# Kernel optimization log

Measured on AMD Instinct MI355X. Metric: run time of the kernel, lower is better.

Reference implementation:

```python
import jax, jax.numpy as jnp
import numpy as np

N_NODES = 50000
N_EDGES = 1600000
IN_CH = 129   # encoding_dim + node_dim
OUT_CH = 64
PERIODS = 25
N_TRAIN = 25000


def setup_inputs() -> dict:
    key = jax.random.key(0)
    ks = jax.random.split(key, 24)
    inp = {
        'x': jax.random.normal(ks[0], (N_NODES, IN_CH, PERIODS), dtype=jnp.float32),
        'edge_index': jax.random.randint(ks[1], (2, N_EDGES), 0, N_NODES, dtype=jnp.int64),
        'y': jax.random.uniform(ks[2], (N_NODES,), dtype=jnp.float32),
        'train_idx': jax.random.randint(ks[3], (N_TRAIN,), 0, N_NODES, dtype=jnp.int64),
    }
    s_in = 1.0 / np.sqrt(IN_CH)
    s_2o = 1.0 / np.sqrt(2 * OUT_CH)
    s_o = 1.0 / np.sqrt(OUT_CH)
    # TGCN gate params: GCNConv weight/bias (IN_CH->OUT_CH), Linear(2*OUT_CH->OUT_CH)
    names = ['z', 'r', 'h']
    for i, g in enumerate(names):
        inp[f'W_{g}'] = jax.random.uniform(ks[4 + 4 * i], (IN_CH, OUT_CH), minval=-s_in, maxval=s_in)
        inp[f'b_{g}'] = jax.random.uniform(ks[5 + 4 * i], (OUT_CH,), minval=-s_in, maxval=s_in)
        inp[f'Wl_{g}'] = jax.random.uniform(ks[6 + 4 * i], (2 * OUT_CH, OUT_CH), minval=-s_2o, maxval=s_2o)
        inp[f'bl_{g}'] = jax.random.uniform(ks[7 + 4 * i], (OUT_CH,), minval=-s_2o, maxval=s_2o)
    inp['attention'] = jax.random.uniform(ks[16], (PERIODS,), dtype=jnp.float32)
    inp['W_o'] = jax.random.uniform(ks[17], (OUT_CH, 1), minval=-s_o, maxval=s_o)
    inp['b_o'] = jax.random.uniform(ks[18], (1,), minval=-s_o, maxval=s_o)
    return inp


def _forward(x, edge_index, y, train_idx, attention,
             W_z, b_z, Wl_z, bl_z, W_r, b_r, Wl_r, bl_r,
             W_h, b_h, Wl_h, bl_h, W_o, b_o):
    N = x.shape[0]
    src, dst = edge_index[0], edge_index[1]
    # GCN symmetric norm with self-loops (edge_weight = 1)
    deg = 1.0 + jax.ops.segment_sum(jnp.ones_like(src, dtype=x.dtype), dst, num_segments=N)
    dinv = jax.lax.rsqrt(deg)
    edge_norm = (dinv[src] * dinv[dst])[:, None]   # (E,1)
    self_norm = (dinv * dinv)[:, None]              # (N,1)

    def gcn(xt, W, b):
        h = xt @ W                                   # (N, OUT_CH)
        agg = jax.ops.segment_sum(edge_norm * h[src], dst, num_segments=N)
        return agg + self_norm * h + b

    probs = jax.nn.softmax(attention)               # (PERIODS,)
    x_seq = jnp.transpose(x, (2, 0, 1))             # (T, N, IN_CH)

    def step(carry, xp):
        H, acc = carry
        xt, p = xp
        Z = jax.nn.sigmoid(jnp.concatenate([gcn(xt, W_z, b_z), H], axis=1) @ Wl_z + bl_z)
        R = jax.nn.sigmoid(jnp.concatenate([gcn(xt, W_r, b_r), H], axis=1) @ Wl_r + bl_r)
        H_tilde = jnp.tanh(jnp.concatenate([gcn(xt, W_h, b_h), H * R], axis=1) @ Wl_h + bl_h)
        H = Z * H + (1.0 - Z) * H_tilde
        return (H, acc + p * H), None

    H0 = jnp.zeros((N, OUT_CH), dtype=x.dtype)
    (H, H_accum), _ = jax.lax.scan(step, (H0, H0), (x_seq, probs))

    out = jax.nn.sigmoid(H_accum @ W_o + b_o)       # (N, 1)
    y_pred = out[:, 0][train_idx]
    return y_pred, y[train_idx]


def reference(x, edge_index, y, train_idx, attention,
              W_z, b_z, Wl_z, bl_z, W_r, b_r, Wl_r, bl_r,
              W_h, b_h, Wl_h, bl_h, W_o, b_o):
    return _forward(x, edge_index, y, train_idx, attention,
                    W_z, b_z, Wl_z, bl_z, W_r, b_r, Wl_r, bl_r,
                    W_h, b_h, Wl_h, bl_h, W_o, b_o)
```

## Files before the change

### kernel.cpp

```cpp
#include <hip/hip_runtime.h>
#include <stdint.h>

#define NND 50000
#define NNDP 50016
#define NE  1600000
#define INC 129
#define TP  25
#define NTR 25000
#define MPAD 50048
#define NC 192
#define NB_SCAN 196
#define CSR_MAX (NE + 8*NND + 128)

typedef short bf16x8 __attribute__((ext_vector_type(8)));
typedef float f32x4 __attribute__((ext_vector_type(4)));
typedef float f32x2 __attribute__((ext_vector_type(2)));

__device__ __forceinline__ uint32_t f2bf(float f){
  union{float ff; uint32_t u;} v; v.ff=f;
  return (v.u + 0x7FFFu + ((v.u>>16)&1u))>>16;
}
__device__ __forceinline__ uint32_t pack2(float a, float b){
  return f2bf(a) | (f2bf(b)<<16);
}
__device__ __forceinline__ float sigm(float v){ return 1.f/(1.f+__expf(-v)); }

__global__ void k_prep(const float* Wz, const float* bz, const float* Wlz, const float* blz,
                       const float* Wr, const float* br, const float* Wlr, const float* blr,
                       const float* Wh, const float* bh, const float* Wlh, const float* blh,
                       uint16_t* BTf, float* ceff, uint16_t* Wlf)
{
  int idx = blockIdx.x*256 + threadIdx.x;
  if (idx < NC*224) {
    int j = idx / 224, k = idx - j*224;
    int g = j >> 6, jj = j & 63;
    const float* W  = g==0?Wz :(g==1?Wr :Wh);
    const float* Wl = g==0?Wlz:(g==1?Wlr:Wlh);
    float v = 0.f;
    if (k < INC) {
      for (int m=0;m<64;m++) v += W[k*64+m]*Wl[m*64+jj];
    } else if (k >= 160) {
      int kk = k-160;
      v = (g<2) ? Wl[(64+kk)*64 + jj] : 0.f;
    }
    int cc = (j>>4)&3, c16 = j&15;
    int kd = k>>1, kk = kd>>4, kgrp = (kd>>2)&3, dw = kd&3, half = k&1;
    int lane = kgrp*16 + c16;
    BTf[(((g*7+kk)*4+cc)*256 + lane*4 + dw)*2 + half] = (uint16_t)f2bf(v);
  } else if (idx < NC*224 + 64*64) {
    int t = idx - NC*224; int j2 = t>>6, k2 = t&63;
    int cc = j2>>4, c16 = j2&15;
    int kd = k2>>1, kk2 = kd>>4, kgrp = (kd>>2)&3, dw = kd&3, half = k2&1;
    int lane = kgrp*16 + c16;
    Wlf[((kk2*4+cc)*256 + lane*4 + dw)*2 + half] = (uint16_t)f2bf(Wlh[(64+k2)*64 + j2]);
  } else if (idx < NC*224 + 64*64 + NC) {
    int j = idx - NC*224 - 64*64;
    int g = j>>6, jj = j&63;
    const float* b  = g==0?bz :(g==1?br :bh);
    const float* Wl = g==0?Wlz:(g==1?Wlr:Wlh);
    const float* bl = g==0?blz:(g==1?blr:blh);
    float v = bl[jj];
    for (int m=0;m<64;m++) v += b[m]*Wl[m*64+jj];
    ceff[j] = v;
  }
}

__global__ void k_probs(const float* att, float* probs){
  if (threadIdx.x==0 && blockIdx.x==0){
    float m=-1e30f;
    for (int i=0;i<TP;i++) m = fmaxf(m, att[i]);
    float e[TP]; float s=0.f;
    for (int i=0;i<TP;i++){ e[i]=__expf(att[i]-m); s+=e[i]; }
    for (int i=0;i<TP;i++) probs[i]=e[i]/s;
  }
}

__global__ void k_hist(const int* eidx, int* deg){
  int e = blockIdx.x*256 + threadIdx.x;
  if (e < NE) atomicAdd(&deg[eidx[NE + e]], 1);
}

__global__ void k_dinv(const int* deg, float* dinv){
  int n = blockIdx.x*256 + threadIdx.x;
  if (n < NND) dinv[n] = rsqrtf(1.0f + (float)deg[n]);
}

__global__ void k_scan1(const int* deg, int* row_ptr, int* bsum){
  __shared__ int s[256];
  int tid = threadIdx.x;
  int i = blockIdx.x*256 + tid;
  int v = (i < NND) ? ((deg[i]+8)&~7) : 0;
  s[tid] = v; __syncthreads();
  for (int d=1; d<256; d<<=1){
    int t = (tid>=d) ? s[tid-d] : 0;
    __syncthreads();
    s[tid] += t; __syncthreads();
  }
  if (i < NND) row_ptr[i] = s[tid] - v;
  if (tid == 255) bsum[blockIdx.x] = s[255];
}
__global__ void k_scan2(int* bsum, int* boff, int* row_ptr){
  __shared__ int s[256];
  int tid = threadIdx.x;
  int v = (tid < NB_SCAN) ? bsum[tid] : 0;
  s[tid] = v; __syncthreads();
  for (int d=1; d<256; d<<=1){
    int t = (tid>=d) ? s[tid-d] : 0;
    __syncthreads();
    s[tid] += t; __syncthreads();
  }
  if (tid < NB_SCAN) boff[tid] = s[tid] - v;
  if (tid == NB_SCAN-1) row_ptr[NND] = s[tid];
}
__global__ void k_scan3(int* row_ptr, const int* boff){
  int i = blockIdx.x*256 + threadIdx.x;
  if (i < NND) row_ptr[i] += boff[blockIdx.x];
}

__global__ void k_fill(const int* eidx, const int* rp, int* cnt, uint16_t* csr){
  int e = blockIdx.x*256 + threadIdx.x;
  if (e < NE){
    int s = eidx[e], d = eidx[NE+e];
    int pos = rp[d] + atomicAdd(&cnt[d],1);
    csr[pos] = (uint16_t)s;
  }
}
__global__ void k_self(const int* rp, const int* deg, uint16_t* csr){
  int n = blockIdx.x*256 + threadIdx.x;
  if (n < NND){
    int base = rp[n] + deg[n];
    int endp = rp[n+1];
    csr[base] = (uint16_t)n;
    for (int j=base+1; j<endp; j++) csr[j] = (uint16_t)NND;
  }
}

__global__ __launch_bounds__(256) void k_transpose3(const float* __restrict__ x,
                                                    const float* __restrict__ dinv,
                                                    uint32_t* __restrict__ xT8,
                                                    float* __restrict__ xsl){
  __shared__ float lx[3232];
  int n = blockIdx.x;
  const float* xr = x + (size_t)n*(INC*TP);
  for (int e=threadIdx.x; e<INC*TP; e+=256) lx[e] = xr[e];
  __syncthreads();
  float dv = dinv[n];
  for (int idx=threadIdx.x; idx<TP*32; idx+=256){
    int t = idx>>5, u = idx&31;
    int c0 = u*4;
    float v0 = lx[(c0+0)*TP+t]*dv, v1 = lx[(c0+1)*TP+t]*dv;
    float v2 = lx[(c0+2)*TP+t]*dv, v3 = lx[(c0+3)*TP+t]*dv;
    int wlo = __builtin_amdgcn_cvt_pk_fp8_f32(v0, v1, 0, false);
    int w   = __builtin_amdgcn_cvt_pk_fp8_f32(v2, v3, wlo, true);
    xT8[((size_t)t*NNDP + n)*32 + u] = (uint32_t)w;
  }
  for (int t=threadIdx.x; t<TP; t+=256)
    xsl[(size_t)t*NNDP + n] = dv*lx[128*TP + t];
  if (blockIdx.x == 0){
    for (int idx=threadIdx.x; idx<TP*32; idx+=256){
      int t = idx>>5, u = idx&31;
      xT8[((size_t)t*NNDP + NND)*32 + u] = 0u;
    }
    for (int t=threadIdx.x; t<TP; t+=256) xsl[(size_t)t*NNDP + NND] = 0.f;
  }
}

__global__ __launch_bounds__(256) void k_agg(const uint16_t* __restrict__ xT8,
    const int* __restrict__ rp, const uint16_t* __restrict__ csr,
    const float* __restrict__ dinv, uint32_t* __restrict__ AX)
{
  int t = blockIdx.y;
  int wave = threadIdx.x>>6, lane = threadIdx.x&63;
  int d = blockIdx.x*4 + wave;
  int beg = __builtin_amdgcn_readfirstlane(rp[d]);
  int end = __builtin_amdgcn_readfirstlane(rp[d+1]);
  const uint16_t* tbl = xT8 + (size_t)t*((size_t)NNDP*64);
  float a0=0.f, a1=0.f;
  for (int i0=beg; i0<end; i0+=8){
    ulonglong2 c = *(const ulonglong2*)(csr + i0);
    #pragma unroll
    for (int k=0;k<4;k++){
      int s0 = (int)((c.x >> (k*16)) & 0xFFFFu);
      int s1 = (int)((c.y >> (k*16)) & 0xFFFFu);
      uint32_t u0 = tbl[(size_t)s0*64 + lane];
      uint32_t u1 = tbl[(size_t)s1*64 + lane];
      f32x2 v0 = __builtin_amdgcn_cvt_pk_f32_fp8((int)u0, false);
      f32x2 v1 = __builtin_amdgcn_cvt_pk_f32_fp8((int)u1, false);
      a0 += v0.x; a1 += v0.y;
      a0 += v1.x; a1 += v1.y;
    }
  }
  float dv = dinv[d];
  AX[(size_t)t*((size_t)MPAD*80) + (size_t)d*80 + lane] = pack2(dv*a0, dv*a1);
}

__global__ void k_aggL(const float* __restrict__ xsl,
    const int* __restrict__ rp, const uint16_t* __restrict__ csr,
    const float* __restrict__ dinv, uint32_t* __restrict__ AX)
{
  int t = blockIdx.y;
  int d = blockIdx.x*256 + threadIdx.x;
  if (d >= NND) return;
  const float* pl = xsl + (size_t)t*NNDP;
  float a = 0.f;
  int beg=rp[d], end=rp[d+1];
  #pragma unroll 4
  for (int i=beg;i<end;i++) a += pl[(int)csr[i]];
  AX[(size_t)t*((size_t)MPAD*80) + (size_t)d*80 + 64] = pack2(dinv[d]*a, 0.f);
}

__global__ __launch_bounds__(256) void k_gru(const uint32_t* __restrict__ AX,
    const uint32_t* __restrict__ BTf, const float* __restrict__ ceff,
    const uint32_t* __restrict__ Wlf, float* __restrict__ accum,
    const float* __restrict__ probs)
{
  __shared__ __align__(16) uint32_t lds4[4*1024];
  int tid = threadIdx.x;
  int wave = tid>>6, lane = tid&63;
  int col16 = lane&15, kgrp = lane>>4;
  uint32_t* myH  = &lds4[wave*1024];
  uint32_t* myHR = &lds4[wave*1024 + 512];
  int n0 = blockIdx.x*64;

  for (int p=lane; p<512; p+=64) myH[p] = 0u;

  float cz[4], cr[4], ch[4];
  #pragma unroll
  for (int cc=0;cc<4;cc++){
    cz[cc] = ceff[cc*16+col16];
    cr[cc] = ceff[64+cc*16+col16];
    ch[cc] = ceff[128+cc*16+col16];
  }

  f32x4 h[4] = {{0,0,0,0},{0,0,0,0},{0,0,0,0},{0,0,0,0}};
  f32x4 acr[4] = {{0,0,0,0},{0,0,0,0},{0,0,0,0},{0,0,0,0}};

  for (int t=0; t<TP; t++){
    const uint32_t* AXrow = AX + (size_t)t*((size_t)MPAD*80)
                               + (size_t)(n0 + wave*16 + col16)*80 + kgrp*4;
    bf16x8 ax[5];
    #pragma unroll
    for (int kk=0; kk<5; kk++) ax[kk] = *(const bf16x8*)(AXrow + kk*16);
    bf16x8 hf0 = *(const bf16x8*)&myH[lane*4];
    bf16x8 hf1 = *(const bf16x8*)&myH[256 + lane*4];

    f32x4 accg[3][4] = {};
    #pragma unroll
    for (int g=0; g<3; g++){
      #pragma unroll
      for (int kk=0; kk<7; kk++){
        bf16x8 a = (kk<5) ? ax[kk] : ((kk==5) ? hf0 : hf1);
        #pragma unroll
        for (int cc=0; cc<4; cc++){
          bf16x8 b = *(const bf16x8*)(BTf + (((g*7+kk)*4+cc)<<8) + lane*4);
          accg[g][cc] = __builtin_amdgcn_mfma_f32_16x16x32_bf16(a,b,accg[g][cc],0,0,0);
        }
      }
    }

    #pragma unroll
    for (int cc=0;cc<4;cc++){
      #pragma unroll
      for (int j=0;j<4;j++){
        float z  = sigm(accg[0][cc][j] + cz[cc]);
        float r  = sigm(accg[1][cc][j] + cr[cc]);
        float ph = accg[2][cc][j] + ch[cc];
        accg[0][cc][j] = z;
        accg[2][cc][j] = ph;
        float hr = h[cc][j]*r;
        float prt = __shfl_xor(hr, 1);
        if (!(col16 & 1)){
          int q = cc*8 + (col16>>1);
          myHR[((q>>4)<<8) + ((((q>>2)&3)*16 + kgrp*4 + j)<<2) + (q&3)] = pack2(hr, prt);
        }
      }
    }

    f32x4 acc2[4] = {};
    #pragma unroll
    for (int kk2=0; kk2<2; kk2++){
      bf16x8 a2 = *(const bf16x8*)&myHR[(kk2<<8) + lane*4];
      #pragma unroll
      for (int cc=0; cc<4; cc++){
        bf16x8 b2 = *(const bf16x8*)(Wlf + (((kk2*4+cc))<<8) + lane*4);
        acc2[cc] = __builtin_amdgcn_mfma_f32_16x16x32_bf16(a2,b2,acc2[cc],0,0,0);
      }
    }

    float pt = probs[t];
    #pragma unroll
    for (int cc=0;cc<4;cc++){
      #pragma unroll
      for (int j=0;j<4;j++){
        float ht = tanhf(acc2[cc][j] + accg[2][cc][j]);
        float z = accg[0][cc][j];
        float hn = z*h[cc][j] + (1.f-z)*ht;
        h[cc][j] = hn;
        acr[cc][j] += pt*hn;
        float prt = __shfl_xor(hn, 1);
        if (!(col16 & 1)){
          int q = cc*8 + (col16>>1);
          myH[((q>>4)<<8) + ((((q>>2)&3)*16 + kgrp*4 + j)<<2) + (q&3)] = pack2(hn, prt);
        }
      }
    }
  }

  #pragma unroll
  for (int cc=0;cc<4;cc++){
    #pragma unroll
    for (int j=0;j<4;j++){
      int n = n0 + wave*16 + kgrp*4 + j;
      if (n < NND)
        accum[(size_t)n*64 + cc*16 + col16] = acr[cc][j];
    }
  }
}

__global__ void k_out(const int* train_idx, const float* accum, const float* Wo,
                      const float* bo, const float* y, float* out){
  int i = blockIdx.x*256 + threadIdx.x;
  if (i < NTR){
    int n = train_idx[i];
    float s = bo[0];
    const float* ar = accum + (size_t)n*64;
    #pragma unroll
    for (int j=0;j<64;j++) s += ar[j]*Wo[j];
    out[i] = sigm(s);
    out[NTR+i] = y[n];
  }
}

extern "C" void kernel_launch(void* const* d_in, const int* in_sizes, int n_in,
                              void* d_out, int out_size, void* d_ws, size_t ws_size,
                              hipStream_t stream)
{
  const float* x   = (const float*)d_in[0];
  const int*   eix = (const int*)d_in[1];
  const float* y   = (const float*)d_in[2];
  const int*   tri = (const int*)d_in[3];
  const float* Wz  = (const float*)d_in[4];
  const float* bz  = (const float*)d_in[5];
  const float* Wlz = (const float*)d_in[6];
  const float* blz = (const float*)d_in[7];
  const float* Wr  = (const float*)d_in[8];
  const float* br  = (const float*)d_in[9];
  const float* Wlr = (const float*)d_in[10];
  const float* blr = (const float*)d_in[11];
  const float* Wh  = (const float*)d_in[12];
  const float* bh  = (const float*)d_in[13];
  const float* Wlh = (const float*)d_in[14];
  const float* blh = (const float*)d_in[15];
  const float* att = (const float*)d_in[16];
  const float* Wo  = (const float*)d_in[17];
  const float* bo  = (const float*)d_in[18];
  float* out = (float*)d_out;

  char* w = (char*)d_ws;
  size_t off = 0;
  auto alloc = [&](size_t sz)->size_t{ size_t o=off; off=(off+sz+255)&~(size_t)255; return o; };

  size_t zo = off;
  size_t o_deg   = alloc((size_t)NND*4);
  size_t o_cnt   = alloc((size_t)NND*4);
  size_t zlen = off - zo;
  size_t o_dinv  = alloc((size_t)NND*4);
  size_t o_rp    = alloc((size_t)(NND+1)*4);
  size_t o_bsum  = alloc((size_t)NB_SCAN*4);
  size_t o_boff  = alloc((size_t)NB_SCAN*4);
  size_t o_csr   = alloc((size_t)CSR_MAX*2);
  size_t o_BT    = alloc((size_t)NC*224*2);
  size_t o_ceff  = alloc((size_t)NC*4);
  size_t o_Wlf   = alloc((size_t)64*64*2);
  size_t o_probs = alloc((size_t)TP*4);
  size_t o_accum = alloc((size_t)MPAD*64*4);
  size_t o_AX    = alloc((size_t)TP*MPAD*80*4);
  size_t o_xT8   = alloc((size_t)TP*NNDP*128);
  size_t o_xl    = alloc((size_t)TP*NNDP*4);
  (void)ws_size; (void)in_sizes; (void)n_in; (void)out_size;

  int*      deg   = (int*)(w+o_deg);
  int*      cnt   = (int*)(w+o_cnt);
  float*    dinv  = (float*)(w+o_dinv);
  int*      rp    = (int*)(w+o_rp);
  int*      bsum  = (int*)(w+o_bsum);
  int*      boff  = (int*)(w+o_boff);
  uint16_t* csr   = (uint16_t*)(w+o_csr);
  uint16_t* BTf   = (uint16_t*)(w+o_BT);
  float*    ceff  = (float*)(w+o_ceff);
  uint16_t* Wlf   = (uint16_t*)(w+o_Wlf);
  float*    probs = (float*)(w+o_probs);
  float*    accum = (float*)(w+o_accum);
  uint32_t* AX    = (uint32_t*)(w+o_AX);
  uint32_t* xT8   = (uint32_t*)(w+o_xT8);
  float*    xsl   = (float*)(w+o_xl);

  hipMemsetAsync(w+zo, 0, zlen, stream);

  k_prep<<<(NC*224 + 64*64 + NC + 255)/256, 256, 0, stream>>>(
      Wz,bz,Wlz,blz, Wr,br,Wlr,blr, Wh,bh,Wlh,blh, BTf, ceff, Wlf);
  k_probs<<<1, 64, 0, stream>>>(att, probs);
  k_hist<<<(NE+255)/256, 256, 0, stream>>>(eix, deg);
  k_dinv<<<(NND+255)/256, 256, 0, stream>>>(deg, dinv);
  k_scan1<<<NB_SCAN, 256, 0, stream>>>(deg, rp, bsum);
  k_scan2<<<1, 256, 0, stream>>>(bsum, boff, rp);
  k_scan3<<<NB_SCAN, 256, 0, stream>>>(rp, boff);
  k_fill<<<(NE+255)/256, 256, 0, stream>>>(eix, rp, cnt, csr);
  k_self<<<NB_SCAN, 256, 0, stream>>>(rp, deg, csr);
  k_transpose3<<<NND, 256, 0, stream>>>(x, dinv, xT8, xsl);

  k_agg <<<dim3(12500, TP), 256, 0, stream>>>((const uint16_t*)xT8, rp, csr, dinv, AX);
  k_aggL<<<dim3(NB_SCAN, TP), 256, 0, stream>>>(xsl, rp, csr, dinv, AX);

  k_gru<<<MPAD/64, 256, 0, stream>>>(AX, (const uint32_t*)BTf, ceff,
                                     (const uint32_t*)Wlf, accum, probs);
  k_out<<<(NTR+255)/256, 256, 0, stream>>>(tri, accum, Wo, bo, y, out);
}
```

Before: 1.932 ms.

## Restructure GRU kernel: transposed MFMA, register shuffles for H, bias folded into GEMM

```diff
diff --git a/kernel.cpp b/kernel.cpp
--- a/kernel.cpp
+++ b/kernel.cpp
@@ -8,13 +8,13 @@
 #define TP  25
 #define NTR 25000
 #define MPAD 50048
-#define NC 192
 #define NB_SCAN 196
 #define CSR_MAX (NE + 8*NND + 128)
 
 typedef short bf16x8 __attribute__((ext_vector_type(8)));
 typedef float f32x4 __attribute__((ext_vector_type(4)));
 typedef float f32x2 __attribute__((ext_vector_type(2)));
+typedef uint32_t u32x4 __attribute__((ext_vector_type(4)));
 
 __device__ __forceinline__ uint32_t f2bf(float f){
   union{float ff; uint32_t u;} v; v.ff=f;
@@ -28,40 +28,36 @@
 __global__ void k_prep(const float* Wz, const float* bz, const float* Wlz, const float* blz,
                        const float* Wr, const float* br, const float* Wlr, const float* blr,
                        const float* Wh, const float* bh, const float* Wlh, const float* blh,
-                       uint16_t* BTf, float* ceff, uint16_t* Wlf)
+                       uint16_t* WfT, uint16_t* Wlf)
 {
   int idx = blockIdx.x*256 + threadIdx.x;
-  if (idx < NC*224) {
+  if (idx < 192*224) {
     int j = idx / 224, k = idx - j*224;
     int g = j >> 6, jj = j & 63;
     const float* W  = g==0?Wz :(g==1?Wr :Wh);
     const float* Wl = g==0?Wlz:(g==1?Wlr:Wlh);
+    const float* b  = g==0?bz :(g==1?br :bh);
+    const float* bl = g==0?blz:(g==1?blr:blh);
     float v = 0.f;
     if (k < INC) {
       for (int m=0;m<64;m++) v += W[k*64+m]*Wl[m*64+jj];
+    } else if (k == 129) {
+      v = bl[jj];
+      for (int m=0;m<64;m++) v += b[m]*Wl[m*64+jj];
     } else if (k >= 160) {
-      int kk = k-160;
-      v = (g<2) ? Wl[(64+kk)*64 + jj] : 0.f;
-    }
-    int cc = (j>>4)&3, c16 = j&15;
-    int kd = k>>1, kk = kd>>4, kgrp = (kd>>2)&3, dw = kd&3, half = k&1;
+      v = (g<2) ? Wl[(64+(k-160))*64 + jj] : 0.f;
+    }
+    int rt = jj>>4, c16 = jj&15;
+    int kk = k>>5, kgrp = (k>>3)&3, e = k&7;
     int lane = kgrp*16 + c16;
-    BTf[(((g*7+kk)*4+cc)*256 + lane*4 + dw)*2 + half] = (uint16_t)f2bf(v);
-  } else if (idx < NC*224 + 64*64) {
-    int t = idx - NC*224; int j2 = t>>6, k2 = t&63;
-    int cc = j2>>4, c16 = j2&15;
-    int kd = k2>>1, kk2 = kd>>4, kgrp = (kd>>2)&3, dw = kd&3, half = k2&1;
+    WfT[((((g*7+kk)*4+rt)*256 + lane*4 + (e>>1))<<1) + (e&1)] = (uint16_t)f2bf(v);
+  } else if (idx < 192*224 + 4096) {
+    int t2 = idx - 192*224; int j2 = t2>>6, k2 = t2&63;
+    float v = Wlh[(64+k2)*64 + j2];
+    int rt = j2>>4, c16 = j2&15;
+    int kk2 = k2>>5, kgrp = (k2>>3)&3, e = k2&7;
     int lane = kgrp*16 + c16;
-    Wlf[((kk2*4+cc)*256 + lane*4 + dw)*2 + half] = (uint16_t)f2bf(Wlh[(64+k2)*64 + j2]);
-  } else if (idx < NC*224 + 64*64 + NC) {
-    int j = idx - NC*224 - 64*64;
-    int g = j>>6, jj = j&63;
-    const float* b  = g==0?bz :(g==1?br :bh);
-    const float* Wl = g==0?Wlz:(g==1?Wlr:Wlh);
-    const float* bl = g==0?blz:(g==1?blr:blh);
-    float v = bl[jj];
-    for (int m=0;m<64;m++) v += b[m]*Wl[m*64+jj];
-    ceff[j] = v;
+    Wlf[(((kk2*4+rt)*256 + lane*4 + (e>>1))<<1) + (e&1)] = (uint16_t)f2bf(v);
   }
 }
 
@@ -206,114 +202,121 @@
   int beg=rp[d], end=rp[d+1];
   #pragma unroll 4
   for (int i=beg;i<end;i++) a += pl[(int)csr[i]];
-  AX[(size_t)t*((size_t)MPAD*80) + (size_t)d*80 + 64] = pack2(dinv[d]*a, 0.f);
-}
-
-__global__ __launch_bounds__(256) void k_gru(const uint32_t* __restrict__ AX,
-    const uint32_t* __restrict__ BTf, const float* __restrict__ ceff,
-    const uint32_t* __restrict__ Wlf, float* __restrict__ accum,
-    const float* __restrict__ probs)
+  AX[(size_t)t*((size_t)MPAD*80) + (size_t)d*80 + 64] = pack2(dinv[d]*a, 1.0f);
+}
+
+__device__ __forceinline__ u32x4 build_frag(uint32_t Pa0, uint32_t Pa1,
+                                            uint32_t Pb0, uint32_t Pb1,
+                                            int srcA, int srcB, bool rsel){
+  uint32_t a0 = (uint32_t)__shfl((int)Pa0, srcA);
+  uint32_t b0 = (uint32_t)__shfl((int)Pb0, srcA);
+  uint32_t a1 = (uint32_t)__shfl((int)Pa1, srcA);
+  uint32_t b1 = (uint32_t)__shfl((int)Pb1, srcA);
+  uint32_t a2 = (uint32_t)__shfl((int)Pa0, srcB);
+  uint32_t b2 = (uint32_t)__shfl((int)Pb0, srcB);
+  uint32_t a3 = (uint32_t)__shfl((int)Pa1, srcB);
+  uint32_t b3 = (uint32_t)__shfl((int)Pb1, srcB);
+  u32x4 o;
+  o.x = rsel?b0:a0; o.y = rsel?b1:a1; o.z = rsel?b2:a2; o.w = rsel?b3:a3;
+  return o;
+}
+
+__global__ __launch_bounds__(64, 3) void k_gru(const uint32_t* __restrict__ AX,
+    const uint32_t* __restrict__ WfT, const uint32_t* __restrict__ Wlf,
+    float* __restrict__ accum, const float* __restrict__ probs)
 {
-  __shared__ __align__(16) uint32_t lds4[4*1024];
-  int tid = threadIdx.x;
-  int wave = tid>>6, lane = tid&63;
-  int col16 = lane&15, kgrp = lane>>4;
-  uint32_t* myH  = &lds4[wave*1024];
-  uint32_t* myHR = &lds4[wave*1024 + 512];
-  int n0 = blockIdx.x*64;
-
-  for (int p=lane; p<512; p+=64) myH[p] = 0u;
-
-  float cz[4], cr[4], ch[4];
-  #pragma unroll
-  for (int cc=0;cc<4;cc++){
-    cz[cc] = ceff[cc*16+col16];
-    cr[cc] = ceff[64+cc*16+col16];
-    ch[cc] = ceff[128+cc*16+col16];
-  }
-
-  f32x4 h[4] = {{0,0,0,0},{0,0,0,0},{0,0,0,0},{0,0,0,0}};
-  f32x4 acr[4] = {{0,0,0,0},{0,0,0,0},{0,0,0,0},{0,0,0,0}};
+  int lane = threadIdx.x & 63;
+  int c16 = lane & 15, q = lane >> 4;
+  int node = blockIdx.x*16 + c16;
+  bool rsel = (q & 2) != 0;
+  int srcA = ((2*q)&3)*16 + c16;
+  int srcB = ((2*q+1)&3)*16 + c16;
+
+  f32x4 h[4] = {};
+  f32x4 acr[4] = {};
+  u32x4 hf0 = {0,0,0,0}, hf1 = {0,0,0,0};
 
   for (int t=0; t<TP; t++){
-    const uint32_t* AXrow = AX + (size_t)t*((size_t)MPAD*80)
-                               + (size_t)(n0 + wave*16 + col16)*80 + kgrp*4;
-    bf16x8 ax[5];
-    #pragma unroll
-    for (int kk=0; kk<5; kk++) ax[kk] = *(const bf16x8*)(AXrow + kk*16);
-    bf16x8 hf0 = *(const bf16x8*)&myH[lane*4];
-    bf16x8 hf1 = *(const bf16x8*)&myH[256 + lane*4];
+    const uint32_t* AXrow = AX + (size_t)t*((size_t)MPAD*80) + (size_t)node*80 + q*4;
+    bf16x8 ax0 = *(const bf16x8*)(AXrow);
+    bf16x8 ax1 = *(const bf16x8*)(AXrow+16);
+    bf16x8 ax2 = *(const bf16x8*)(AXrow+32);
+    bf16x8 ax3 = *(const bf16x8*)(AXrow+48);
+    bf16x8 ax4 = *(const bf16x8*)(AXrow+64);
 
     f32x4 accg[3][4] = {};
     #pragma unroll
-    for (int g=0; g<3; g++){
+    for (int kk=0; kk<7; kk++){
+      bf16x8 xv;
+      if      (kk==0) xv = ax0;
+      else if (kk==1) xv = ax1;
+      else if (kk==2) xv = ax2;
+      else if (kk==3) xv = ax3;
+      else if (kk==4) xv = ax4;
+      else if (kk==5) xv = __builtin_bit_cast(bf16x8, hf0);
+      else            xv = __builtin_bit_cast(bf16x8, hf1);
       #pragma unroll
-      for (int kk=0; kk<7; kk++){
-        bf16x8 a = (kk<5) ? ax[kk] : ((kk==5) ? hf0 : hf1);
+      for (int g=0; g<3; g++){
+        if (g==2 && kk>=5) continue;
         #pragma unroll
-        for (int cc=0; cc<4; cc++){
-          bf16x8 b = *(const bf16x8*)(BTf + (((g*7+kk)*4+cc)<<8) + lane*4);
-          accg[g][cc] = __builtin_amdgcn_mfma_f32_16x16x32_bf16(a,b,accg[g][cc],0,0,0);
+        for (int rt=0; rt<4; rt++){
+          bf16x8 wv = *(const bf16x8*)(WfT + (((g*7+kk)*4+rt)<<8) + lane*4);
+          accg[g][rt] = __builtin_amdgcn_mfma_f32_16x16x32_bf16(wv, xv, accg[g][rt],0,0,0);
         }
       }
     }
 
-    #pragma unroll
-    for (int cc=0;cc<4;cc++){
+    uint32_t Phr[4][2];
+    #pragma unroll
+    for (int rt=0; rt<4; rt++){
+      float hrv[4];
       #pragma unroll
       for (int j=0;j<4;j++){
-        float z  = sigm(accg[0][cc][j] + cz[cc]);
-        float r  = sigm(accg[1][cc][j] + cr[cc]);
-        float ph = accg[2][cc][j] + ch[cc];
-        accg[0][cc][j] = z;
-        accg[2][cc][j] = ph;
-        float hr = h[cc][j]*r;
-        float prt = __shfl_xor(hr, 1);
-        if (!(col16 & 1)){
-          int q = cc*8 + (col16>>1);
-          myHR[((q>>4)<<8) + ((((q>>2)&3)*16 + kgrp*4 + j)<<2) + (q&3)] = pack2(hr, prt);
-        }
+        float z = sigm(accg[0][rt][j]);
+        float r = sigm(accg[1][rt][j]);
+        accg[0][rt][j] = z;
+        hrv[j] = h[rt][j]*r;
       }
-    }
+      Phr[rt][0] = pack2(hrv[0], hrv[1]);
+      Phr[rt][1] = pack2(hrv[2], hrv[3]);
+    }
+    u32x4 hrf0 = build_frag(Phr[0][0],Phr[0][1],Phr[1][0],Phr[1][1], srcA,srcB,rsel);
+    u32x4 hrf1 = build_frag(Phr[2][0],Phr[2][1],Phr[3][0],Phr[3][1], srcA,srcB,rsel);
 
     f32x4 acc2[4] = {};
     #pragma unroll
     for (int kk2=0; kk2<2; kk2++){
-      bf16x8 a2 = *(const bf16x8*)&myHR[(kk2<<8) + lane*4];
+      bf16x8 bv = __builtin_bit_cast(bf16x8, kk2 ? hrf1 : hrf0);
       #pragma unroll
-      for (int cc=0; cc<4; cc++){
-        bf16x8 b2 = *(const bf16x8*)(Wlf + (((kk2*4+cc))<<8) + lane*4);
-        acc2[cc] = __builtin_amdgcn_mfma_f32_16x16x32_bf16(a2,b2,acc2[cc],0,0,0);
+      for (int rt=0; rt<4; rt++){
+        bf16x8 wv = *(const bf16x8*)(Wlf + ((kk2*4+rt)<<8) + lane*4);
+        acc2[rt] = __builtin_amdgcn_mfma_f32_16x16x32_bf16(wv, bv, acc2[rt],0,0,0);
       }
     }
 
     float pt = probs[t];
-    #pragma unroll
-    for (int cc=0;cc<4;cc++){
+    uint32_t Ph[4][2];
+    #pragma unroll
+    for (int rt=0; rt<4; rt++){
       #pragma unroll
       for (int j=0;j<4;j++){
-        float ht = tanhf(acc2[cc][j] + accg[2][cc][j]);
-        float z = accg[0][cc][j];
-        float hn = z*h[cc][j] + (1.f-z)*ht;
-        h[cc][j] = hn;
-        acr[cc][j] += pt*hn;
-        float prt = __shfl_xor(hn, 1);
-        if (!(col16 & 1)){
-          int q = cc*8 + (col16>>1);
-          myH[((q>>4)<<8) + ((((q>>2)&3)*16 + kgrp*4 + j)<<2) + (q&3)] = pack2(hn, prt);
-        }
+        float ht = tanhf(acc2[rt][j] + accg[2][rt][j]);
+        float z  = accg[0][rt][j];
+        float hn = z*h[rt][j] + (1.f-z)*ht;
+        h[rt][j] = hn;
+        acr[rt][j] += pt*hn;
       }
-    }
-  }
-
-  #pragma unroll
-  for (int cc=0;cc<4;cc++){
-    #pragma unroll
-    for (int j=0;j<4;j++){
-      int n = n0 + wave*16 + kgrp*4 + j;
-      if (n < NND)
-        accum[(size_t)n*64 + cc*16 + col16] = acr[cc][j];
-    }
+      Ph[rt][0] = pack2(h[rt][0], h[rt][1]);
+      Ph[rt][1] = pack2(h[rt][2], h[rt][3]);
+    }
+    hf0 = build_frag(Ph[0][0],Ph[0][1],Ph[1][0],Ph[1][1], srcA,srcB,rsel);
+    hf1 = build_frag(Ph[2][0],Ph[2][1],Ph[3][0],Ph[3][1], srcA,srcB,rsel);
+  }
+
+  if (node < NND){
+    #pragma unroll
+    for (int rt=0; rt<4; rt++)
+      *(f32x4*)&accum[(size_t)node*64 + rt*16 + q*4] = acr[rt];
   }
 }
 
@@ -369,9 +372,8 @@
   size_t o_bsum  = alloc((size_t)NB_SCAN*4);
   size_t o_boff  = alloc((size_t)NB_SCAN*4);
   size_t o_csr   = alloc((size_t)CSR_MAX*2);
-  size_t o_BT    = alloc((size_t)NC*224*2);
-  size_t o_ceff  = alloc((size_t)NC*4);
-  size_t o_Wlf   = alloc((size_t)64*64*2);
+  size_t o_WfT   = alloc((size_t)84*512*2);
+  size_t o_Wlf   = alloc((size_t)8*512*2);
   size_t o_probs = alloc((size_t)TP*4);
   size_t o_accum = alloc((size_t)MPAD*64*4);
   size_t o_AX    = alloc((size_t)TP*MPAD*80*4);
@@ -386,8 +388,7 @@
   int*      bsum  = (int*)(w+o_bsum);
   int*      boff  = (int*)(w+o_boff);
   uint16_t* csr   = (uint16_t*)(w+o_csr);
-  uint16_t* BTf   = (uint16_t*)(w+o_BT);
-  float*    ceff  = (float*)(w+o_ceff);
+  uint16_t* WfT   = (uint16_t*)(w+o_WfT);
   uint16_t* Wlf   = (uint16_t*)(w+o_Wlf);
   float*    probs = (float*)(w+o_probs);
   float*    accum = (float*)(w+o_accum);
@@ -397,8 +398,8 @@
 
   hipMemsetAsync(w+zo, 0, zlen, stream);
 
-  k_prep<<<(NC*224 + 64*64 + NC + 255)/256, 256, 0, stream>>>(
-      Wz,bz,Wlz,blz, Wr,br,Wlr,blr, Wh,bh,Wlh,blh, BTf, ceff, Wlf);
+  k_prep<<<(192*224 + 4096 + 255)/256, 256, 0, stream>>>(
+      Wz,bz,Wlz,blz, Wr,br,Wlr,blr, Wh,bh,Wlh,blh, WfT, Wlf);
   k_probs<<<1, 64, 0, stream>>>(att, probs);
   k_hist<<<(NE+255)/256, 256, 0, stream>>>(eix, deg);
   k_dinv<<<(NND+255)/256, 256, 0, stream>>>(deg, dinv);
@@ -412,7 +413,7 @@
   k_agg <<<dim3(12500, TP), 256, 0, stream>>>((const uint16_t*)xT8, rp, csr, dinv, AX);
   k_aggL<<<dim3(NB_SCAN, TP), 256, 0, stream>>>(xsl, rp, csr, dinv, AX);
 
-  k_gru<<<MPAD/64, 256, 0, stream>>>(AX, (const uint32_t*)BTf, ceff,
-                                     (const uint32_t*)Wlf, accum, probs);
+  k_gru<<<MPAD/16, 64, 0, stream>>>(AX, (const uint32_t*)WfT,
+                                    (const uint32_t*)Wlf, accum, probs);
   k_out<<<(NTR+255)/256, 256, 0, stream>>>(tri, accum, Wo, bo, y, out);
 }
```

Result: slower. 2.636 ms (+36.4%).
